# Kernel tuning notes

Measured on AMD Instinct MI355X. Metric: run time of the kernel, lower is better.

The kernel has to match this reference:

```python
import jax, jax.numpy as jnp
import numpy as np

ALPHA = 0.3

def setup_inputs() -> dict:
    key = jax.random.key(0)
    x = jax.random.normal(key, (4096, 64, 256), dtype=jnp.float32)
    return {"x": x}

def reference(x) -> jnp.ndarray:
    # EWMA: y[0] = x[0]; y[t] = alpha*x[t] + (1-alpha)*y[t-1]
    alpha = jnp.asarray(ALPHA, x.dtype)
    one_m_alpha = jnp.asarray(1.0 - ALPHA, x.dtype)

    def step(carry, xt):
        yt = alpha * xt + one_m_alpha * carry
        return yt, yt

    y0 = x[0]
    _, ys = jax.lax.scan(step, y0, x[1:])
    return jnp.concatenate([y0[None], ys], axis=0)
```

## Files before the change

### kernel.cpp

```cpp
#include <hip/hip_runtime.h>


#define A_COEF 0.3f
#define B_COEF 0.7f

typedef float vfloat4 __attribute__((ext_vector_type(4)));

constexpr int T  = 4096;
constexpr int C4 = 4096;
constexpr int L  = 128;
constexpr int W  = 32;

__global__ __launch_bounds__(256) void ewma_kernel(const vfloat4* __restrict__ x,
                                                   vfloat4* __restrict__ y) {
    const int c  = blockIdx.x * 256 + threadIdx.x;
    const int k  = blockIdx.y;
    const int t0 = k * L;

    vfloat4 carry;
    int t;
    if (k == 0) {
        carry = x[c];
        __builtin_nontemporal_store(carry, &y[c]);
        t = 1;
    } else {
        const int ts = t0 - W;
        carry = x[(size_t)ts * C4 + c];
        #pragma unroll 8
        for (int tt = ts + 1; tt < t0; ++tt) {
            vfloat4 v = x[(size_t)tt * C4 + c];
            carry = A_COEF * v + B_COEF * carry;
        }
        t = t0;
    }

    const int tend = t0 + L;
    #pragma unroll 8
    for (; t < tend; ++t) {
        const size_t idx = (size_t)t * C4 + c;
        vfloat4 v = x[idx];
        carry = A_COEF * v + B_COEF * carry;
        __builtin_nontemporal_store(carry, &y[idx]);
    }
}

extern "C" void kernel_launch(void* const* d_in, const int* in_sizes, int n_in,
                              void* d_out, int out_size, void* d_ws, size_t ws_size,
                              hipStream_t stream) {
    const vfloat4* x = (const vfloat4*)d_in[0];
    vfloat4*       y = (vfloat4*)d_out;
    dim3 grid(C4 / 256, T / L);
    ewma_kernel<<<grid, 256, 0, stream>>>(x, y);
}
```

Baseline: 455.9 us.

## Software-pipeline EWMA loads with register double buffering and pointer increments

Restructures the main time loop so the next group of 8 timesteps is loaded into registers while the current group is computed and stored, keeping more loads in flight per thread. It also fully unrolls the warm-up loop, switches to incremental pointer arithmetic, and replaces nontemporal stores with plain stores. The k==0 case now recomputes the first element through the common path. The cost is extra register pressure, and the store change may alter cache behaviour.

```diff
diff --git a/kernel.cpp b/kernel.cpp
--- a/kernel.cpp
+++ b/kernel.cpp
@@ -10,6 +10,7 @@
 constexpr int C4 = 4096;
 constexpr int L  = 128;
 constexpr int W  = 32;
+constexpr int PF = 8;
 
 __global__ __launch_bounds__(256) void ewma_kernel(const vfloat4* __restrict__ x,
                                                    vfloat4* __restrict__ y) {
@@ -18,29 +19,49 @@
     const int t0 = k * L;
 
     vfloat4 carry;
-    int t;
     if (k == 0) {
         carry = x[c];
-        __builtin_nontemporal_store(carry, &y[c]);
-        t = 1;
     } else {
-        const int ts = t0 - W;
-        carry = x[(size_t)ts * C4 + c];
-        #pragma unroll 8
-        for (int tt = ts + 1; tt < t0; ++tt) {
-            vfloat4 v = x[(size_t)tt * C4 + c];
+        const vfloat4* p = x + (size_t)(t0 - W) * C4 + c;
+        carry = *p;
+        #pragma unroll
+        for (int i = 1; i < W; ++i) {
+            p += C4;
+            vfloat4 v = *p;
             carry = A_COEF * v + B_COEF * carry;
         }
-        t = t0;
     }
 
-    const int tend = t0 + L;
-    #pragma unroll 8
-    for (; t < tend; ++t) {
-        const size_t idx = (size_t)t * C4 + c;
-        vfloat4 v = x[idx];
-        carry = A_COEF * v + B_COEF * carry;
-        __builtin_nontemporal_store(carry, &y[idx]);
+    const vfloat4* pl = x + (size_t)t0 * C4 + c;
+    vfloat4*       ps = y + (size_t)t0 * C4 + c;
+
+    vfloat4 buf[PF];
+    #pragma unroll
+    for (int i = 0; i < PF; ++i) buf[i] = pl[(size_t)i * C4];
+    pl += (size_t)PF * C4;
+
+    #pragma unroll 1
+    for (int g = 0; g < L / PF - 1; ++g) {
+        vfloat4 nxt[PF];
+        #pragma unroll
+        for (int i = 0; i < PF; ++i) nxt[i] = pl[(size_t)i * C4];
+        pl += (size_t)PF * C4;
+
+        #pragma unroll
+        for (int i = 0; i < PF; ++i) {
+            carry = A_COEF * buf[i] + B_COEF * carry;
+            ps[(size_t)i * C4] = carry;
+        }
+        ps += (size_t)PF * C4;
+
+        #pragma unroll
+        for (int i = 0; i < PF; ++i) buf[i] = nxt[i];
+    }
+
+    #pragma unroll
+    for (int i = 0; i < PF; ++i) {
+        carry = A_COEF * buf[i] + B_COEF * carry;
+        ps[(size_t)i * C4] = carry;
     }
 }
 
```

Measured after the change: 455.4 us. About the same (-0.1%).
